# Performance work log

Hardware: AMD Instinct MI355X
Metric: run time of the kernel (lower is better)

## Reference

```python
import jax, jax.numpy as jnp
import numpy as np

D_MODEL = 1024
N_HEADS = 16
D_K = D_MODEL // N_HEADS
B, S = 2, 2048


def setup_inputs() -> dict:
    key = jax.random.key(0)
    ks = jax.random.split(key, 12)
    scale = 1.0 / np.sqrt(D_MODEL)
    inp = {
        "query": jax.random.normal(ks[0], (B, S, D_MODEL), jnp.float32),
        "key": jax.random.normal(ks[1], (B, S, D_MODEL), jnp.float32),
        "value": jax.random.normal(ks[2], (B, S, D_MODEL), jnp.float32),
        "mask": jnp.tril(jnp.ones((S, S), dtype=bool))[None, None],  # (1,1,S,S) causal
        "W_q": jax.random.normal(ks[3], (D_MODEL, D_MODEL), jnp.float32) * scale,
        "b_q": jnp.zeros((D_MODEL,), jnp.float32),
        "W_k": jax.random.normal(ks[4], (D_MODEL, D_MODEL), jnp.float32) * scale,
        "b_k": jnp.zeros((D_MODEL,), jnp.float32),
        "W_v": jax.random.normal(ks[5], (D_MODEL, D_MODEL), jnp.float32) * scale,
        "b_v": jnp.zeros((D_MODEL,), jnp.float32),
        "W_o": jax.random.normal(ks[6], (D_MODEL, D_MODEL), jnp.float32) * scale,
        "b_o": jnp.zeros((D_MODEL,), jnp.float32),
    }
    return inp


def reference(query, key, value, mask, W_q, b_q, W_k, b_k, W_v, b_v, W_o, b_o):
    b = query.shape[0]
    # Linear projections (torch Linear: x @ W.T + b), split into heads -> (b,h,s,d_k)
    def proj(x, W, bias):
        y = x @ W.T + bias
        return y.reshape(b, -1, N_HEADS, D_K).transpose(0, 2, 1, 3)

    q = proj(query, W_q, b_q)
    k = proj(key, W_k, b_k)
    v = proj(value, W_v, b_v)

    # scores: (b,h,sq,sk)
    scores = jnp.einsum("bhqd,bhkd->bhqk", q, k) / jnp.sqrt(jnp.float32(D_K)).astype(q.dtype)
    scores = jnp.where(mask, scores, jnp.finfo(scores.dtype).min)
    attn = jax.nn.softmax(scores, axis=-1)
    out = jnp.einsum("bhqk,bhkd->bhqd", attn, v)  # (b,h,sq,d_k)
    out = out.transpose(0, 2, 1, 3).reshape(b, -1, D_MODEL)
    return out @ W_o.T + b_o
```

## Files before the change

### kernel.cpp

```cpp
#include <hip/hip_runtime.h>
#include <hip/hip_bf16.h>
#include <stdint.h>

#define D_MODEL 1024
#define NH 16
#define DK 64
#define BB 2
#define SS 2048
#define MROWS (BB*SS)

typedef __attribute__((ext_vector_type(8))) short bf16x8;
typedef __attribute__((ext_vector_type(4))) float f32x4;

__device__ __forceinline__ short to_bf16(float f) {
  __hip_bfloat16 h = __float2bfloat16(f);
  union { __hip_bfloat16 b; short s; } u; u.b = h; return u.s;
}

__device__ __forceinline__ f32x4 mfma16(bf16x8 a, bf16x8 b, f32x4 c) {
  return __builtin_amdgcn_mfma_f32_16x16x32_bf16(a, b, c, 0, 0, 0);
}

__device__ __forceinline__ void gload_lds16(const void* g, void* l) {
  __builtin_amdgcn_global_load_lds(
      (const __attribute__((address_space(1))) unsigned int*)g,
      (__attribute__((address_space(3))) unsigned int*)l,
      16, 0, 0);
}

__global__ __launch_bounds__(256) void cvt3(const float* __restrict__ a,
                                            const float* __restrict__ b,
                                            const float* __restrict__ c,
                                            short* __restrict__ oa,
                                            short* __restrict__ ob,
                                            short* __restrict__ oc) {
  const int z = blockIdx.z;
  const float* x = z == 0 ? a : z == 1 ? b : c;
  short* y = z == 0 ? oa : z == 1 ? ob : oc;
  const int i = (blockIdx.x * 256 + threadIdx.x) * 4;
  const float4 v = *(const float4*)(x + i);
  short4 o;
  o.x = to_bf16(v.x); o.y = to_bf16(v.y); o.z = to_bf16(v.z); o.w = to_bf16(v.w);
  *(short4*)(y + i) = o;
}

__global__ __launch_bounds__(256) void cvt4(const float* __restrict__ a,
                                            const float* __restrict__ b,
                                            const float* __restrict__ c,
                                            const float* __restrict__ d,
                                            short* __restrict__ oa,
                                            short* __restrict__ ob,
                                            short* __restrict__ oc,
                                            short* __restrict__ od) {
  const int z = blockIdx.z;
  const float* x = z == 0 ? a : z == 1 ? b : z == 2 ? c : d;
  short* y = z == 0 ? oa : z == 1 ? ob : z == 2 ? oc : od;
  const int i = (blockIdx.x * 256 + threadIdx.x) * 4;
  const float4 v = *(const float4*)(x + i);
  short4 o;
  o.x = to_bf16(v.x); o.y = to_bf16(v.y); o.z = to_bf16(v.z); o.w = to_bf16(v.w);
  *(short4*)(y + i) = o;
}

__global__ __launch_bounds__(256) void gemm_qkv(const short* __restrict__ Xq,
                                                const short* __restrict__ Xk,
                                                const short* __restrict__ Xv,
                                                const short* __restrict__ Wq,
                                                const short* __restrict__ Wk,
                                                const short* __restrict__ Wv,
                                                const float* __restrict__ bq,
                                                const float* __restrict__ bk,
                                                const float* __restrict__ bv,
                                                short* __restrict__ Qh,
                                                short* __restrict__ Kh,
                                                short* __restrict__ VT) {
  constexpr int K = 1024;
  __shared__ short As[128 * 64];
  __shared__ short Bs[128 * 64];
  const int z = blockIdx.z;
  const short* A    = z == 0 ? Xq : z == 1 ? Xk : Xv;
  const short* Wt   = z == 0 ? Wq : z == 1 ? Wk : Wv;
  const float* bias = z == 0 ? bq : z == 1 ? bk : bv;

  const int tid = threadIdx.x;
  const int w = tid >> 6, lane = tid & 63;
  const int m0 = blockIdx.x * 128, n0 = blockIdx.y * 128;
  const int wm = w >> 1, wn = w & 1;
  const int fr = lane & 15, fg = lane >> 4;
  const int srow = tid >> 3, scol = (tid & 7) * 8;

  f32x4 acc[4][4] = {};

  for (int k0 = 0; k0 < K; k0 += 64) {
    __syncthreads();
#pragma unroll
    for (int i = 0; i < 4; ++i) {
      const int row = i * 32 + srow;
      gload_lds16(A  + (size_t)(m0 + row) * K + k0 + scol, As + row * 64 + scol);
      gload_lds16(Wt + (size_t)(n0 + row) * K + k0 + scol, Bs + row * 64 + scol);
    }
    asm volatile("s_waitcnt vmcnt(0)" ::: "memory");
    __syncthreads();

    bf16x8 af[4][2], bfr[4][2];
#pragma unroll
    for (int i = 0; i < 4; ++i)
#pragma unroll
      for (int hh = 0; hh < 2; ++hh) {
        af[i][hh]  = *(const bf16x8*)(As + (wm * 64 + i * 16 + fr) * 64 + hh * 32 + fg * 8);
        bfr[i][hh] = *(const bf16x8*)(Bs + (wn * 64 + i * 16 + fr) * 64 + hh * 32 + fg * 8);
      }
    __builtin_amdgcn_s_setprio(1);
#pragma unroll
    for (int mi = 0; mi < 4; ++mi)
#pragma unroll
      for (int ni = 0; ni < 4; ++ni) {
        acc[mi][ni] = mfma16(af[mi][0], bfr[ni][0], acc[mi][ni]);
        acc[mi][ni] = mfma16(af[mi][1], bfr[ni][1], acc[mi][ni]);
      }
    __builtin_amdgcn_s_setprio(0);
  }

  const float scale = (z == 0) ? 0.18033688011112042f : 1.0f;
#pragma unroll
  for (int mi = 0; mi < 4; ++mi)
#pragma unroll
    for (int ni = 0; ni < 4; ++ni) {
      const int col = n0 + wn * 64 + ni * 16 + fr;
      const float bval = bias[col];
      const int h = col >> 6, d = col & 63;
#pragma unroll
      for (int r = 0; r < 4; ++r) {
        const int row = m0 + wm * 64 + mi * 16 + fg * 4 + r;
        const float val = (acc[mi][ni][r] + bval) * scale;
        const int b = row >> 11, s = row & (SS - 1);
        if (z < 2) {
          short* dst = (z == 0) ? Qh : Kh;
          dst[((size_t)(b * NH + h) * SS + s) * DK + d] = to_bf16(val);
        } else {
          VT[((size_t)(b * NH + h) * DK + d) * SS + s] = to_bf16(val);
        }
      }
    }
}

__global__ __launch_bounds__(256) void gemm_out(const short* __restrict__ A,
                                                const short* __restrict__ Wt,
                                                const float* __restrict__ bias,
                                                float* __restrict__ Y) {
  constexpr int K = 1024;
  __shared__ short As[128 * 64];
  __shared__ short Bs[64 * 64];
  const int tid = threadIdx.x;
  const int w = tid >> 6, lane = tid & 63;
  const int m0 = blockIdx.x * 128, n0 = blockIdx.y * 64;
  const int wm = w >> 1, wn = w & 1;
  const int fr = lane & 15, fg = lane >> 4;
  const int srow = tid >> 3, scol = (tid & 7) * 8;

  f32x4 acc[4][2] = {};

  for (int k0 = 0; k0 < K; k0 += 64) {
    __syncthreads();
#pragma unroll
    for (int i = 0; i < 4; ++i) {
      const int row = i * 32 + srow;
      gload_lds16(A + (size_t)(m0 + row) * K + k0 + scol, As + row * 64 + scol);
    }
#pragma unroll
    for (int i = 0; i < 2; ++i) {
      const int row = i * 32 + srow;
      gload_lds16(Wt + (size_t)(n0 + row) * K + k0 + scol, Bs + row * 64 + scol);
    }
    asm volatile("s_waitcnt vmcnt(0)" ::: "memory");
    __syncthreads();

    bf16x8 af[4][2], bfr[2][2];
#pragma unroll
    for (int i = 0; i < 4; ++i)
#pragma unroll
      for (int hh = 0; hh < 2; ++hh)
        af[i][hh] = *(const bf16x8*)(As + (wm * 64 + i * 16 + fr) * 64 + hh * 32 + fg * 8);
#pragma unroll
    for (int i = 0; i < 2; ++i)
#pragma unroll
      for (int hh = 0; hh < 2; ++hh)
        bfr[i][hh] = *(const bf16x8*)(Bs + (wn * 32 + i * 16 + fr) * 64 + hh * 32 + fg * 8);
    __builtin_amdgcn_s_setprio(1);
#pragma unroll
    for (int mi = 0; mi < 4; ++mi)
#pragma unroll
      for (int ni = 0; ni < 2; ++ni) {
        acc[mi][ni] = mfma16(af[mi][0], bfr[ni][0], acc[mi][ni]);
        acc[mi][ni] = mfma16(af[mi][1], bfr[ni][1], acc[mi][ni]);
      }
    __builtin_amdgcn_s_setprio(0);
  }

#pragma unroll
  for (int mi = 0; mi < 4; ++mi)
#pragma unroll
    for (int ni = 0; ni < 2; ++ni) {
      const int col = n0 + wn * 32 + ni * 16 + fr;
      const float bval = bias[col];
#pragma unroll
      for (int r = 0; r < 4; ++r) {
        const int row = m0 + wm * 64 + mi * 16 + fg * 4 + r;
        Y[(size_t)row * D_MODEL + col] = acc[mi][ni][r] + bval;
      }
    }
}

__global__ __launch_bounds__(256) void attn_kernel(const short* __restrict__ Qh,
                                                   const short* __restrict__ Kh,
                                                   const short* __restrict__ VT,
                                                   short* __restrict__ AO) {
  __shared__ short Ks[2][64 * 64];
  __shared__ short Vs[2][64 * 64];
  __shared__ short P_lds[4][16 * 64];

  const int tid = threadIdx.x, w = tid >> 6, lane = tid & 63;
  const int fr = lane & 15, fg = lane >> 4;
  const int kr = fg * 4;
  const int swz = (fr & 7) << 4;

  const int bid = blockIdx.x;
  const int lid = ((bid & 7) << 6) | (bid >> 3);
  const int bh = lid >> 4;
  const int j = lid & 15;
  const int b = bh >> 4, h = bh & 15;

  const short* Qp = Qh + (size_t)bh * SS * DK;
  const short* Kp = Kh + (size_t)bh * SS * DK;
  const short* Vp = VT + (size_t)bh * DK * SS;

  const int sc_c = tid & 7;
  const int sc_r = tid >> 3;

  const int T0 = j + 1;

  int qw = j * 64 + w * 16;
  bf16x8 qf[2];
#pragma unroll
  for (int hh = 0; hh < 2; ++hh)
    qf[hh] = *(const bf16x8*)(Qp + (size_t)(qw + fr) * DK + hh * 32 + fg * 8);

  const short onev = (fr == 0) ? (short)0x3F80 : (short)0;
  const bf16x8 af4 = {onev, onev, onev, onev, onev, onev, onev, onev};

  f32x4 o[5] = {};
  float m_run = -1e30f;

#define STAGE_KV(buf, kk0)                                                    \
  do {                                                                        \
    _Pragma("unroll") for (int p = 0; p < 2; ++p) {                           \
      const int row = p * 32 + sc_r;                                          \
      const int sc = sc_c ^ (row & 7);                                        \
      gload_lds16(Kp + (size_t)((kk0) + row) * DK + sc * 8,                   \
                  &Ks[buf][row * 64 + sc_c * 8]);                             \
      gload_lds16(Vp + (size_t)row * SS + (kk0) + sc * 8,                     \
                  &Vs[buf][row * 64 + sc_c * 8]);                             \
    }                                                                         \
  } while (0)

  STAGE_KV(0, 0);
  asm volatile("s_waitcnt vmcnt(0)" ::: "memory");
  __syncthreads();

  for (int g = 0; g < 33; ++g) {
    const int cur = g & 1;
    if (g + 1 < 33) {
      const int nk0 = (g + 1 < T0) ? (g + 1) * 64 : (g + 1 - T0) * 64;
      STAGE_KV(cur ^ 1, nk0);
    }

    const char* KsB = (const char*)Ks[cur];
    const char* VsB = (const char*)Vs[cur];

    f32x4 st[4];
    __builtin_amdgcn_s_setprio(1);
#pragma unroll
    for (int kt = 0; kt < 4; ++kt) {
      const bf16x8 k0f = *(const bf16x8*)(KsB + (kt * 16 + fr) * 128 + ((fg * 16) ^ swz));
      const bf16x8 k1f = *(const bf16x8*)(KsB + (kt * 16 + fr) * 128 + ((64 + fg * 16) ^ swz));
      f32x4 z = {};
      z = mfma16(k0f, qf[0], z);
      z = mfma16(k1f, qf[1], z);
      st[kt] = z;
    }
    __builtin_amdgcn_s_setprio(0);

    if (g == T0 - 1 || g == 32) {
#pragma unroll
      for (int kt = 0; kt < 4; ++kt)
#pragma unroll
        for (int r = 0; r < 4; ++r)
          if (kt * 16 + kr + r > w * 16 + fr) st[kt][r] = -1e30f;
    }

    float pmax = st[0][0];
#pragma unroll
    for (int kt = 0; kt < 4; ++kt)
#pragma unroll
      for (int r = 0; r < 4; ++r) pmax = fmaxf(pmax, st[kt][r]);
    pmax = fmaxf(pmax, __shfl_xor(pmax, 16));
    pmax = fmaxf(pmax, __shfl_xor(pmax, 32));

    if (!__all(pmax <= m_run + 11.0f)) {
      const float mn = fmaxf(m_run, pmax);
      const float al = __builtin_amdgcn_exp2f(m_run - mn);
      m_run = mn;
#pragma unroll
      for (int t = 0; t < 5; ++t)
#pragma unroll
        for (int r = 0; r < 4; ++r) o[t][r] *= al;
    }

    {
      char* base = (char*)P_lds[w];
#pragma unroll
      for (int kt = 0; kt < 4; ++kt) {
        short4 sv;
        sv.x = to_bf16(__builtin_amdgcn_exp2f(st[kt][0] - m_run));
        sv.y = to_bf16(__builtin_amdgcn_exp2f(st[kt][1] - m_run));
        sv.z = to_bf16(__builtin_amdgcn_exp2f(st[kt][2] - m_run));
        sv.w = to_bf16(__builtin_amdgcn_exp2f(st[kt][3] - m_run));
        *(short4*)(base + ((fr * 128 + kt * 32 + fg * 8) ^ swz)) = sv;
      }
    }
    asm volatile("s_waitcnt lgkmcnt(0)" ::: "memory");

    __builtin_amdgcn_s_setprio(1);
#pragma unroll
    for (int c = 0; c < 2; ++c) {
      const bf16x8 pf = *(const bf16x8*)((const char*)P_lds[w] +
                                         ((fr * 128 + c * 64 + fg * 16) ^ swz));
#pragma unroll
      for (int t = 0; t < 4; ++t) {
        const bf16x8 vfb = *(const bf16x8*)(VsB + (t * 16 + fr) * 128 +
                                            ((c * 64 + fg * 16) ^ swz));
        o[t] = mfma16(vfb, pf, o[t]);
      }
      o[4] = mfma16(af4, pf, o[4]);
    }
    __builtin_amdgcn_s_setprio(0);

    asm volatile("s_waitcnt vmcnt(0)" ::: "memory");
    __syncthreads();

    if (g == T0 - 1) {
      const float l = __shfl(o[4][0], fr);
      const float inv = 1.0f / l;
      const int s = qw + fr;
#pragma unroll
      for (int t = 0; t < 4; ++t) {
        short4 ov = {to_bf16(o[t][0] * inv), to_bf16(o[t][1] * inv),
                     to_bf16(o[t][2] * inv), to_bf16(o[t][3] * inv)};
        *(short4*)(AO + (size_t)(b * SS + s) * D_MODEL + h * 64 + t * 16 + kr) = ov;
      }
#pragma unroll
      for (int t = 0; t < 5; ++t)
#pragma unroll
        for (int r = 0; r < 4; ++r) o[t][r] = 0.f;
      m_run = -1e30f;
      qw = (31 - j) * 64 + w * 16;
#pragma unroll
      for (int hh = 0; hh < 2; ++hh)
        qf[hh] = *(const bf16x8*)(Qp + (size_t)(qw + fr) * DK + hh * 32 + fg * 8);
    }
  }
#undef STAGE_KV

  const float l = __shfl(o[4][0], fr);
  const float inv = 1.0f / l;
  const int s = qw + fr;
#pragma unroll
  for (int t = 0; t < 4; ++t) {
    short4 ov = {to_bf16(o[t][0] * inv), to_bf16(o[t][1] * inv),
                 to_bf16(o[t][2] * inv), to_bf16(o[t][3] * inv)};
    *(short4*)(AO + (size_t)(b * SS + s) * D_MODEL + h * 64 + t * 16 + kr) = ov;
  }
}

extern "C" void kernel_launch(void* const* d_in, const int* in_sizes, int n_in,
                              void* d_out, int out_size, void* d_ws, size_t ws_size,
                              hipStream_t stream) {
  const float* q  = (const float*)d_in[0];
  const float* k  = (const float*)d_in[1];
  const float* v  = (const float*)d_in[2];
  const float* Wq = (const float*)d_in[4];
  const float* bq = (const float*)d_in[5];
  const float* Wk = (const float*)d_in[6];
  const float* bk = (const float*)d_in[7];
  const float* Wv = (const float*)d_in[8];
  const float* bv = (const float*)d_in[9];
  const float* Wo = (const float*)d_in[10];
  const float* bo = (const float*)d_in[11];

  char* ws = (char*)d_ws;
  const size_t MB = 1u << 20;
  short* Xq = (short*)(ws + 0 * MB);
  short* Xk = (short*)(ws + 8 * MB);
  short* Xv = (short*)(ws + 16 * MB);
  short* Bq = (short*)(ws + 24 * MB);
  short* Bk = (short*)(ws + 26 * MB);
  short* Bv = (short*)(ws + 28 * MB);
  short* Bo = (short*)(ws + 30 * MB);
  short* Qh = (short*)(ws + 32 * MB);
  short* Kh = (short*)(ws + 40 * MB);
  short* VT = (short*)(ws + 48 * MB);
  short* AO = (short*)(ws + 56 * MB);

  cvt3<<<dim3(MROWS * D_MODEL / 1024, 1, 3), 256, 0, stream>>>(q, k, v, Xq, Xk, Xv);
  cvt4<<<dim3(D_MODEL * D_MODEL / 1024, 1, 4), 256, 0, stream>>>(Wq, Wk, Wv, Wo, Bq, Bk, Bv, Bo);

  gemm_qkv<<<dim3(MROWS / 128, D_MODEL / 128, 3), 256, 0, stream>>>(
      Xq, Xk, Xv, Bq, Bk, Bv, bq, bk, bv, Qh, Kh, VT);

  attn_kernel<<<dim3(512), 256, 0, stream>>>(Qh, Kh, VT, AO);

  gemm_out<<<dim3(MROWS / 128, D_MODEL / 64), 256, 0, stream>>>(AO, Bo, bo, (float*)d_out);
}
```

Baseline: 126.2 us.

## Software-pipeline attention: overlap QK^T of next tile with softmax/PV of previous

Restructures the attention loop into a two-stage software pipeline: iteration g computes QK^T scores for tile g while running softmax and the PV MMA for tile g-1. K/V staging moves to a triple-buffered LDS ring with a prefetch distance of two. The row-max reduction also switches to a max3 tree. The aim is to overlap MFMA score work with exp/softmax VALU work and hide global-load latency, at the cost of more LDS, more live score registers, and extra logic at the causal segment boundary.

```diff
diff --git a/kernel.cpp b/kernel.cpp
--- a/kernel.cpp
+++ b/kernel.cpp
@@ -26,6 +26,10 @@
       (const __attribute__((address_space(1))) unsigned int*)g,
       (__attribute__((address_space(3))) unsigned int*)l,
       16, 0, 0);
+}
+
+__device__ __forceinline__ float max3f(float a, float b, float c) {
+  return fmaxf(fmaxf(a, b), c);
 }
 
 __global__ __launch_bounds__(256) void cvt3(const float* __restrict__ a,
@@ -215,8 +219,8 @@
                                                    const short* __restrict__ Kh,
                                                    const short* __restrict__ VT,
                                                    short* __restrict__ AO) {
-  __shared__ short Ks[2][64 * 64];
-  __shared__ short Vs[2][64 * 64];
+  __shared__ short Ks[3][64 * 64];
+  __shared__ short Vs[3][64 * 64];
   __shared__ short P_lds[4][16 * 64];
 
   const int tid = threadIdx.x, w = tid >> 6, lane = tid & 63;
@@ -239,18 +243,19 @@
 
   const int T0 = j + 1;
 
-  int qw = j * 64 + w * 16;
   bf16x8 qf[2];
 #pragma unroll
   for (int hh = 0; hh < 2; ++hh)
-    qf[hh] = *(const bf16x8*)(Qp + (size_t)(qw + fr) * DK + hh * 32 + fg * 8);
+    qf[hh] = *(const bf16x8*)(Qp + (size_t)(j * 64 + w * 16 + fr) * DK + hh * 32 + fg * 8);
 
   const short onev = (fr == 0) ? (short)0x3F80 : (short)0;
   const bf16x8 af4 = {onev, onev, onev, onev, onev, onev, onev, onev};
 
   f32x4 o[5] = {};
   float m_run = -1e30f;
-
+  f32x4 stA[4], stB[4];
+
+#define KK0(g) ((((g) < T0) ? (g) : ((g) - T0)) * 64)
 #define STAGE_KV(buf, kk0)                                                    \
   do {                                                                        \
     _Pragma("unroll") for (int p = 0; p < 2; ++p) {                           \
@@ -263,46 +268,13 @@
     }                                                                         \
   } while (0)
 
-  STAGE_KV(0, 0);
-  asm volatile("s_waitcnt vmcnt(0)" ::: "memory");
-  __syncthreads();
-
-  for (int g = 0; g < 33; ++g) {
-    const int cur = g & 1;
-    if (g + 1 < 33) {
-      const int nk0 = (g + 1 < T0) ? (g + 1) * 64 : (g + 1 - T0) * 64;
-      STAGE_KV(cur ^ 1, nk0);
-    }
-
-    const char* KsB = (const char*)Ks[cur];
-    const char* VsB = (const char*)Vs[cur];
-
-    f32x4 st[4];
-    __builtin_amdgcn_s_setprio(1);
-#pragma unroll
-    for (int kt = 0; kt < 4; ++kt) {
-      const bf16x8 k0f = *(const bf16x8*)(KsB + (kt * 16 + fr) * 128 + ((fg * 16) ^ swz));
-      const bf16x8 k1f = *(const bf16x8*)(KsB + (kt * 16 + fr) * 128 + ((64 + fg * 16) ^ swz));
-      f32x4 z = {};
-      z = mfma16(k0f, qf[0], z);
-      z = mfma16(k1f, qf[1], z);
-      st[kt] = z;
-    }
-    __builtin_amdgcn_s_setprio(0);
-
-    if (g == T0 - 1 || g == 32) {
-#pragma unroll
-      for (int kt = 0; kt < 4; ++kt)
-#pragma unroll
-        for (int r = 0; r < 4; ++r)
-          if (kt * 16 + kr + r > w * 16 + fr) st[kt][r] = -1e30f;
-    }
-
-    float pmax = st[0][0];
-#pragma unroll
-    for (int kt = 0; kt < 4; ++kt)
-#pragma unroll
-      for (int r = 0; r < 4; ++r) pmax = fmaxf(pmax, st[kt][r]);
+  auto softmax_pv = [&](int bufPrev) {
+    float p0 = max3f(stB[0][0], stB[0][1], stB[0][2]);
+    float p1 = max3f(stB[0][3], stB[1][0], stB[1][1]);
+    float p2 = max3f(stB[1][2], stB[1][3], stB[2][0]);
+    float p3 = max3f(stB[2][1], stB[2][2], stB[2][3]);
+    float p4 = max3f(stB[3][0], stB[3][1], stB[3][2]);
+    float pmax = fmaxf(max3f(p0, p1, p2), max3f(p3, p4, stB[3][3]));
     pmax = fmaxf(pmax, __shfl_xor(pmax, 16));
     pmax = fmaxf(pmax, __shfl_xor(pmax, 32));
 
@@ -316,20 +288,19 @@
         for (int r = 0; r < 4; ++r) o[t][r] *= al;
     }
 
-    {
-      char* base = (char*)P_lds[w];
-#pragma unroll
-      for (int kt = 0; kt < 4; ++kt) {
-        short4 sv;
-        sv.x = to_bf16(__builtin_amdgcn_exp2f(st[kt][0] - m_run));
-        sv.y = to_bf16(__builtin_amdgcn_exp2f(st[kt][1] - m_run));
-        sv.z = to_bf16(__builtin_amdgcn_exp2f(st[kt][2] - m_run));
-        sv.w = to_bf16(__builtin_amdgcn_exp2f(st[kt][3] - m_run));
-        *(short4*)(base + ((fr * 128 + kt * 32 + fg * 8) ^ swz)) = sv;
-      }
+    char* base = (char*)P_lds[w];
+#pragma unroll
+    for (int kt = 0; kt < 4; ++kt) {
+      short4 sv;
+      sv.x = to_bf16(__builtin_amdgcn_exp2f(stB[kt][0] - m_run));
+      sv.y = to_bf16(__builtin_amdgcn_exp2f(stB[kt][1] - m_run));
+      sv.z = to_bf16(__builtin_amdgcn_exp2f(stB[kt][2] - m_run));
+      sv.w = to_bf16(__builtin_amdgcn_exp2f(stB[kt][3] - m_run));
+      *(short4*)(base + ((fr * 128 + kt * 32 + fg * 8) ^ swz)) = sv;
     }
     asm volatile("s_waitcnt lgkmcnt(0)" ::: "memory");
 
+    const char* VsB = (const char*)Vs[bufPrev];
     __builtin_amdgcn_s_setprio(1);
 #pragma unroll
     for (int c = 0; c < 2; ++c) {
@@ -344,42 +315,78 @@
       o[4] = mfma16(af4, pf, o[4]);
     }
     __builtin_amdgcn_s_setprio(0);
+  };
+
+  auto store_o = [&](int qbase) {
+    const float l = __shfl(o[4][0], fr);
+    const float inv = 1.0f / l;
+    const int s = qbase + w * 16 + fr;
+#pragma unroll
+    for (int t = 0; t < 4; ++t) {
+      short4 ov = {to_bf16(o[t][0] * inv), to_bf16(o[t][1] * inv),
+                   to_bf16(o[t][2] * inv), to_bf16(o[t][3] * inv)};
+      *(short4*)(AO + (size_t)(b * SS + s) * D_MODEL + h * 64 + t * 16 + kr) = ov;
+    }
+  };
+
+  STAGE_KV(0, 0);
+  STAGE_KV(1, KK0(1));
+  asm volatile("s_waitcnt vmcnt(0)" ::: "memory");
+  __syncthreads();
+
+  for (int g = 0; g < 33; ++g) {
+    if (g == T0) {
+#pragma unroll
+      for (int hh = 0; hh < 2; ++hh)
+        qf[hh] = *(const bf16x8*)(Qp + (size_t)((31 - j) * 64 + w * 16 + fr) * DK + hh * 32 + fg * 8);
+    }
+
+    {
+      const char* KsB = (const char*)Ks[g % 3];
+      __builtin_amdgcn_s_setprio(1);
+#pragma unroll
+      for (int kt = 0; kt < 4; ++kt) {
+        const bf16x8 k0f = *(const bf16x8*)(KsB + (kt * 16 + fr) * 128 + ((fg * 16) ^ swz));
+        const bf16x8 k1f = *(const bf16x8*)(KsB + (kt * 16 + fr) * 128 + ((64 + fg * 16) ^ swz));
+        f32x4 z = {};
+        z = mfma16(k0f, qf[0], z);
+        z = mfma16(k1f, qf[1], z);
+        stA[kt] = z;
+      }
+      __builtin_amdgcn_s_setprio(0);
+    }
+    if (g == T0 - 1 || g == 32) {
+#pragma unroll
+      for (int kt = 0; kt < 4; ++kt)
+#pragma unroll
+        for (int r = 0; r < 4; ++r)
+          if (kt * 16 + kr + r > w * 16 + fr) stA[kt][r] = -1e30f;
+    }
+
+    if (g > 0) {
+      softmax_pv((g - 1) % 3);
+      if (g == T0) {
+        store_o(j * 64);
+#pragma unroll
+        for (int t = 0; t < 5; ++t)
+#pragma unroll
+          for (int r = 0; r < 4; ++r) o[t][r] = 0.f;
+        m_run = -1e30f;
+      }
+    }
+
+#pragma unroll
+    for (int kt = 0; kt < 4; ++kt) stB[kt] = stA[kt];
 
     asm volatile("s_waitcnt vmcnt(0)" ::: "memory");
     __syncthreads();
-
-    if (g == T0 - 1) {
-      const float l = __shfl(o[4][0], fr);
-      const float inv = 1.0f / l;
-      const int s = qw + fr;
-#pragma unroll
-      for (int t = 0; t < 4; ++t) {
-        short4 ov = {to_bf16(o[t][0] * inv), to_bf16(o[t][1] * inv),
-                     to_bf16(o[t][2] * inv), to_bf16(o[t][3] * inv)};
-        *(short4*)(AO + (size_t)(b * SS + s) * D_MODEL + h * 64 + t * 16 + kr) = ov;
-      }
-#pragma unroll
-      for (int t = 0; t < 5; ++t)
-#pragma unroll
-        for (int r = 0; r < 4; ++r) o[t][r] = 0.f;
-      m_run = -1e30f;
-      qw = (31 - j) * 64 + w * 16;
-#pragma unroll
-      for (int hh = 0; hh < 2; ++hh)
-        qf[hh] = *(const bf16x8*)(Qp + (size_t)(qw + fr) * DK + hh * 32 + fg * 8);
-    }
+    if (g + 2 <= 32) STAGE_KV((g + 2) % 3, KK0(g + 2));
   }
+
+  softmax_pv(32 % 3);
+  store_o((31 - j) * 64);
 #undef STAGE_KV
-
-  const float l = __shfl(o[4][0], fr);
-  const float inv = 1.0f / l;
-  const int s = qw + fr;
-#pragma unroll
-  for (int t = 0; t < 4; ++t) {
-    short4 ov = {to_bf16(o[t][0] * inv), to_bf16(o[t][1] * inv),
-                 to_bf16(o[t][2] * inv), to_bf16(o[t][3] * inv)};
-    *(short4*)(AO + (size_t)(b * SS + s) * D_MODEL + h * 64 + t * 16 + kr) = ov;
-  }
+#undef KK0
 }
 
 extern "C" void kernel_launch(void* const* d_in, const int* in_sizes, int n_in,
```

Result: no change. 123.7 us (-1.9%).
